# Optimization experiments

Measured on AMD Instinct MI355X. Metric: run time of the kernel, lower is better.

The kernel has to match this reference:

```python
import jax, jax.numpy as jnp
import numpy as np

B, S, D = 4, 4096, 2048
H, HD = 16, 128
FFN = 8192
CAP = 0.25
TOP_K = int(S * CAP)  # 1024
EPS = 1e-6


def rmsnorm(x, g):
    return x * jax.lax.rsqrt(jnp.mean(x * x, axis=-1, keepdims=True) + EPS) * g


def apply_rope(x, cos, sin):
    # x: [b,t,h,hd]; cos/sin: [t, hd//2]
    half = x.shape[-1] // 2
    x1, x2 = x[..., :half], x[..., half:]
    c = cos[None, :, None, :]
    s = sin[None, :, None, :]
    return jnp.concatenate([x1 * c - x2 * s, x1 * s + x2 * c], axis=-1)


def transformer_block(x, mask, freqs_cis, g1, wq, wk, wv, wo, g2, w1, w3, w2):
    b, t, d = x.shape
    cos, sin = freqs_cis[..., 0], freqs_cis[..., 1]
    h = rmsnorm(x, g1)
    q = (h @ wq).reshape(b, t, H, HD)
    k = (h @ wk).reshape(b, t, H, HD)
    v = (h @ wv).reshape(b, t, H, HD)
    q = apply_rope(q, cos, sin)
    k = apply_rope(k, cos, sin)
    scores = jnp.einsum('bqhd,bkhd->bhqk', q, k) / np.sqrt(HD) + mask[None, None]
    attn = jax.nn.softmax(scores, axis=-1)
    o = jnp.einsum('bhqk,bkhd->bqhd', attn, v).reshape(b, t, d) @ wo
    x = x + o
    h2 = rmsnorm(x, g2)
    x = x + (jax.nn.silu(h2 @ w1) * (h2 @ w3)) @ w2
    return x, None


def setup_inputs() -> dict:
    key = jax.random.key(0)
    ks = jax.random.split(key, 12)
    w = lambda k, shp: jax.random.normal(k, shp, dtype=jnp.float32) * 0.02
    return {
        'x': jax.random.normal(ks[0], (B, S, D), dtype=jnp.float32),
        'mask': jnp.zeros((TOP_K, TOP_K), dtype=jnp.float32),
        'freqs_cis': jax.random.uniform(ks[1], (TOP_K, HD // 2, 2), dtype=jnp.float32),
        'w_router': w(ks[2], (D,)),
        'g1': jnp.ones((D,), dtype=jnp.float32),
        'wq': w(ks[3], (D, D)),
        'wk': w(ks[4], (D, D)),
        'wv': w(ks[5], (D, D)),
        'wo': w(ks[6], (D, D)),
        'g2': jnp.ones((D,), dtype=jnp.float32),
        'w1': w(ks[7], (D, FFN)),
        'w3': w(ks[8], (D, FFN)),
        'w2': w(ks[9], (FFN, D)),
    }


def reference(x, mask, freqs_cis, w_router, g1, wq, wk, wv, wo, g2, w1, w3, w2):
    b, s, d = x.shape
    # router: Linear(dim, 1, bias=False) -> [b, s]
    router_logits = jnp.einsum('bsd,d->bs', x, w_router)
    vals, idx = jax.lax.top_k(router_logits, TOP_K)  # [b, k]
    # sort selected indices ascending; permute weights to match (softmax is
    # permutation-equivariant so softmax-then-permute == torch's gather order)
    order = jnp.argsort(idx, axis=1)
    sel = jnp.take_along_axis(idx, order, axis=1)          # [b, k]
    w_sel = jnp.take_along_axis(vals, order, axis=1)       # [b, k]
    r_weights = jax.nn.softmax(w_sel, axis=1)[..., None]   # [b, k, 1]
    filtered_x = jnp.take_along_axis(x, sel[..., None], axis=1)  # [b, k, d]
    x_out, _ = transformer_block(filtered_x, mask, freqs_cis, g1, wq, wk, wv, wo, g2, w1, w3, w2)
    xw_out = r_weights * x_out
    b_idx = jnp.arange(b)[:, None]
    out = x.at[b_idx, sel].add(xw_out)
    return out
```

## Files before the change

kernel.cpp:

```cpp
#include <hip/hip_runtime.h>
#include <cstdint>
#include <cstddef>

#define NB 4
#define NS 4096
#define ND 2048
#define NH 16
#define NHD 128
#define NT 1024
#define NF 8192

typedef __bf16 bf16;
typedef __bf16 bf16x8 __attribute__((ext_vector_type(8)));
typedef __bf16 bf16x4 __attribute__((ext_vector_type(4)));
typedef float  f32x4  __attribute__((ext_vector_type(4)));

typedef const __attribute__((address_space(1))) void* gptr_t;
typedef __attribute__((address_space(3))) void* lptr_t;

__device__ __forceinline__ float wave_sum(float v) {
#pragma unroll
    for (int off = 32; off > 0; off >>= 1) v += __shfl_xor(v, off);
    return v;
}
__device__ __forceinline__ float wave_max(float v) {
#pragma unroll
    for (int off = 32; off > 0; off >>= 1) v = fmaxf(v, __shfl_xor(v, off));
    return v;
}

__global__ __launch_bounds__(256) void router_k(const float* __restrict__ x,
                                                const float* __restrict__ wr,
                                                float* __restrict__ logits) {
    __shared__ float r4[4];
    long long row = blockIdx.x;
    const float4* xr = (const float4*)(x + row * ND);
    const float4* w4 = (const float4*)wr;
    float p = 0.f;
    for (int i = threadIdx.x; i < ND / 4; i += 256) {
        float4 a = xr[i], b = w4[i];
        p += a.x * b.x + a.y * b.y + a.z * b.z + a.w * b.w;
    }
    p = wave_sum(p);
    if ((threadIdx.x & 63) == 0) r4[threadIdx.x >> 6] = p;
    __syncthreads();
    if (threadIdx.x == 0) logits[row] = r4[0] + r4[1] + r4[2] + r4[3];
}

__global__ __launch_bounds__(1024) void topk_k(const float* __restrict__ logits,
                                               int* __restrict__ sel,
                                               float* __restrict__ rw) {
    __shared__ unsigned long long keys[NS];
    __shared__ float r16[16];
    __shared__ float bmax, bsum;
    const int bb = blockIdx.x;
    const int tid = threadIdx.x;
    const float* lg = logits + (long long)bb * NS;

    for (int i = tid; i < NS; i += 1024) {
        unsigned u = __float_as_uint(lg[i]);
        u = (u & 0x80000000u) ? ~u : (u | 0x80000000u);
        keys[i] = ((unsigned long long)u << 32) | (unsigned)(NS - 1 - i);
    }
    __syncthreads();
    for (int k = 2; k <= NS; k <<= 1) {
        for (int j = k >> 1; j > 0; j >>= 1) {
            for (int i = tid; i < NS; i += 1024) {
                int ixj = i ^ j;
                if (ixj > i) {
                    unsigned long long a = keys[i], c = keys[ixj];
                    bool up = ((i & k) == 0);
                    if (up ? (a < c) : (a > c)) { keys[i] = c; keys[ixj] = a; }
                }
            }
            __syncthreads();
        }
    }
    unsigned long long a0 = keys[tid];
    __syncthreads();
    {
        unsigned idx_ = NS - 1 - (unsigned)(a0 & 0xFFFFFFFFu);
        unsigned uval = (unsigned)(a0 >> 32);
        keys[tid] = ((unsigned long long)idx_ << 32) | uval;
    }
    __syncthreads();
    for (int k = 2; k <= NT; k <<= 1) {
        for (int j = k >> 1; j > 0; j >>= 1) {
            int i = tid, ixj = i ^ j;
            if (i < NT && ixj > i) {
                unsigned long long a = keys[i], c = keys[ixj];
                bool up = ((i & k) == 0);
                if (up ? (a > c) : (a < c)) { keys[i] = c; keys[ixj] = a; }
            }
            __syncthreads();
        }
    }
    unsigned long long kk = keys[tid];
    int si = (int)(kk >> 32);
    unsigned u = (unsigned)(kk & 0xFFFFFFFFu);
    u = (u & 0x80000000u) ? (u ^ 0x80000000u) : ~u;
    float val = __uint_as_float(u);

    const int wid = tid >> 6, lane = tid & 63;
    float mx = wave_max(val);
    if (lane == 0) r16[wid] = mx;
    __syncthreads();
    if (tid == 0) {
        float m = r16[0];
        for (int i = 1; i < 16; i++) m = fmaxf(m, r16[i]);
        bmax = m;
    }
    __syncthreads();
    float e = __expf(val - bmax);
    float s = wave_sum(e);
    if (lane == 0) r16[wid] = s;
    __syncthreads();
    if (tid == 0) {
        float t = 0.f;
        for (int i = 0; i < 16; i++) t += r16[i];
        bsum = t;
    }
    __syncthreads();
    sel[bb * NT + tid] = si;
    rw[bb * NT + tid] = e / bsum;
}

__global__ __launch_bounds__(256) void gather_k(const float* __restrict__ x,
                                                const int* __restrict__ sel,
                                                float* __restrict__ xf) {
    int gid = blockIdx.x * 256 + threadIdx.x;
    int col = gid & (ND / 4 - 1);
    int row = gid >> 9;
    int bb = row >> 10;
    int s = sel[row];
    ((float4*)xf)[gid] = ((const float4*)x)[((long long)bb * NS + s) * (ND / 4) + col];
}

__global__ __launch_bounds__(256) void rmsnorm_k(const float* __restrict__ x,
                                                 const float* __restrict__ g,
                                                 bf16* __restrict__ out) {
    __shared__ float r4[4];
    __shared__ float scl;
    long long row = blockIdx.x;
    const float4* xr = (const float4*)(x + row * ND);
    int i0 = threadIdx.x, i1 = threadIdx.x + 256;
    float4 a = xr[i0], b = xr[i1];
    float ss = a.x * a.x + a.y * a.y + a.z * a.z + a.w * a.w +
               b.x * b.x + b.y * b.y + b.z * b.z + b.w * b.w;
    ss = wave_sum(ss);
    if ((threadIdx.x & 63) == 0) r4[threadIdx.x >> 6] = ss;
    __syncthreads();
    if (threadIdx.x == 0)
        scl = rsqrtf((r4[0] + r4[1] + r4[2] + r4[3]) * (1.0f / ND) + 1e-6f);
    __syncthreads();
    float s = scl;
    const float4* g4 = (const float4*)g;
    float4 ga = g4[i0], gb = g4[i1];
    bf16x4 o0, o1;
    o0[0] = (bf16)(a.x * s * ga.x); o0[1] = (bf16)(a.y * s * ga.y);
    o0[2] = (bf16)(a.z * s * ga.z); o0[3] = (bf16)(a.w * s * ga.w);
    o1[0] = (bf16)(b.x * s * gb.x); o1[1] = (bf16)(b.y * s * gb.y);
    o1[2] = (bf16)(b.z * s * gb.z); o1[3] = (bf16)(b.w * s * gb.w);
    *(bf16x4*)(out + row * ND + i0 * 4) = o0;
    *(bf16x4*)(out + row * ND + i1 * 4) = o1;
}

__global__ __launch_bounds__(256) void transpose_to_bf16(const float* __restrict__ in,
                                                         bf16* __restrict__ out,
                                                         int R, int C) {
    __shared__ float tile[32][33];
    int bx = blockIdx.x * 32;
    int by = blockIdx.y * 32;
    int tx = threadIdx.x & 31;
    int ty = threadIdx.x >> 5;
#pragma unroll
    for (int i = 0; i < 4; i++)
        tile[ty + 8 * i][tx] = in[(long long)(by + ty + 8 * i) * C + bx + tx];
    __syncthreads();
#pragma unroll
    for (int i = 0; i < 4; i++)
        out[(long long)(bx + ty + 8 * i) * R + by + tx] = (bf16)tile[tx][ty + 8 * i];
}

__global__ __launch_bounds__(256) void rope_k(const bf16* __restrict__ QKV,
                                              const float* __restrict__ fr,
                                              bf16* __restrict__ Q,
                                              bf16* __restrict__ K,
                                              bf16* __restrict__ Vt) {
    int gid = blockIdx.x * 256 + threadIdx.x;
    int hd = gid & 63;
    int h = (gid >> 6) & 15;
    int t = (gid >> 10) & (NT - 1);
    int bb = gid >> 20;
    float c = fr[t * 128 + hd * 2 + 0];
    float s = fr[t * 128 + hd * 2 + 1];
    long long base = ((long long)bb * NT + t) * (3 * ND) + h * NHD;
    float q1 = (float)QKV[base + hd],      q2 = (float)QKV[base + hd + 64];
    float k1 = (float)QKV[base + ND + hd], k2 = (float)QKV[base + ND + hd + 64];
    long long ob = (((long long)(bb * NH + h)) * NT + t) * NHD;
    Q[ob + hd]      = (bf16)(q1 * c - q2 * s);
    Q[ob + hd + 64] = (bf16)(q1 * s + q2 * c);
    K[ob + hd]      = (bf16)(k1 * c - k2 * s);
    K[ob + hd + 64] = (bf16)(k1 * s + k2 * c);
    long long vb = ((long long)(bb * NH + h)) * NHD * NT + t;
    Vt[vb + (long long)hd * NT]        = QKV[base + 2 * ND + hd];
    Vt[vb + (long long)(hd + 64) * NT] = QKV[base + 2 * ND + hd + 64];
}

__global__ __launch_bounds__(256) void softmax_k(const float* __restrict__ Sc,
                                                 bf16* __restrict__ P) {
    __shared__ float r4[4];
    __shared__ float bc;
    long long row = blockIdx.x;
    float4 v = ((const float4*)(Sc + row * NT))[threadIdx.x];
    float mx = fmaxf(fmaxf(v.x, v.y), fmaxf(v.z, v.w));
    mx = wave_max(mx);
    if ((threadIdx.x & 63) == 0) r4[threadIdx.x >> 6] = mx;
    __syncthreads();
    if (threadIdx.x == 0) bc = fmaxf(fmaxf(r4[0], r4[1]), fmaxf(r4[2], r4[3]));
    __syncthreads();
    float m = bc;
    float e0 = __expf(v.x - m), e1 = __expf(v.y - m);
    float e2 = __expf(v.z - m), e3 = __expf(v.w - m);
    float ss = wave_sum(e0 + e1 + e2 + e3);
    if ((threadIdx.x & 63) == 0) r4[threadIdx.x >> 6] = ss;
    __syncthreads();
    if (threadIdx.x == 0) bc = 1.f / (r4[0] + r4[1] + r4[2] + r4[3]);
    __syncthreads();
    float inv = bc;
    bf16x4 o;
    o[0] = (bf16)(e0 * inv); o[1] = (bf16)(e1 * inv);
    o[2] = (bf16)(e2 * inv); o[3] = (bf16)(e3 * inv);
    *(bf16x4*)(P + row * NT + threadIdx.x * 4) = o;
}

__global__ __launch_bounds__(256) void copy_k(const float4* __restrict__ in,
                                              float4* __restrict__ out, long long n) {
    for (long long i = (long long)blockIdx.x * 256 + threadIdx.x; i < n;
         i += (long long)gridDim.x * 256)
        out[i] = in[i];
}

template <int MODE>
__global__ __launch_bounds__(256, 2) void gemm_bt(
    const bf16* __restrict__ A, int lda, long long sAz,
    const bf16* __restrict__ Bt, int ldb, long long sBz,
    void* __restrict__ Cv, long long sCz, int ldc,
    int K, float alpha) {
    __shared__ bf16 As[128][32];
    __shared__ bf16 Bs[128][32];

    const int tid = threadIdx.x;
    const int lane = tid & 63;
    const int wave = tid >> 6;
    const int wm = wave >> 1, wn = wave & 1;
    const int lm = lane & 15, lq = lane >> 4;

    const int m0 = blockIdx.y * 128;
    const int n0 = blockIdx.x * 128;
    const int z = blockIdx.z;

    A += (long long)z * sAz;
    Bt += (long long)z * sBz;

    f32x4 acc[4][4];
#pragma unroll
    for (int i = 0; i < 4; i++)
#pragma unroll
        for (int j = 0; j < 4; j++) {
            f32x4 zz = {0.f, 0.f, 0.f, 0.f};
            acc[i][j] = zz;
        }

    const int sr = wave * 16 + (lane >> 2);
    const int sk = (lane & 3) * 8;
    const bf16* gA0 = A + (long long)(m0 + sr) * lda + sk;
    const bf16* gA1 = gA0 + (long long)64 * lda;
    const bf16* gB0 = Bt + (long long)(n0 + sr) * ldb + sk;
    const bf16* gB1 = gB0 + (long long)64 * ldb;
    bf16* lA0 = &As[sr][sk];
    bf16* lA1 = &As[sr + 64][sk];
    bf16* lB0 = &Bs[sr][sk];
    bf16* lB1 = &Bs[sr + 64][sk];

    for (int k0 = 0; k0 < K; k0 += 32) {
        __builtin_amdgcn_global_load_lds((gptr_t)(gA0 + k0), (lptr_t)lA0, 16, 0, 0);
        __builtin_amdgcn_global_load_lds((gptr_t)(gA1 + k0), (lptr_t)lA1, 16, 0, 0);
        __builtin_amdgcn_global_load_lds((gptr_t)(gB0 + k0), (lptr_t)lB0, 16, 0, 0);
        __builtin_amdgcn_global_load_lds((gptr_t)(gB1 + k0), (lptr_t)lB1, 16, 0, 0);
        __syncthreads();

        bf16x8 af[4], bfr[4];
#pragma unroll
        for (int mi = 0; mi < 4; mi++)
            af[mi] = *(const bf16x8*)&As[wm * 64 + mi * 16 + lm][lq * 8];
#pragma unroll
        for (int ni = 0; ni < 4; ni++)
            bfr[ni] = *(const bf16x8*)&Bs[wn * 64 + ni * 16 + lm][lq * 8];
#pragma unroll
        for (int mi = 0; mi < 4; mi++)
#pragma unroll
            for (int ni = 0; ni < 4; ni++)
                acc[mi][ni] = __builtin_amdgcn_mfma_f32_16x16x32_bf16(
                    af[mi], bfr[ni], acc[mi][ni], 0, 0, 0);
        __syncthreads();
    }

#pragma unroll
    for (int mi = 0; mi < 4; mi++) {
#pragma unroll
        for (int ni = 0; ni < 4; ni++) {
            int row = m0 + wm * 64 + mi * 16 + lq * 4;
            int col = n0 + wn * 64 + ni * 16 + lm;
#pragma unroll
            for (int r = 0; r < 4; r++) {
                float v = alpha * acc[mi][ni][r];
                long long rr = row + r;
                if constexpr (MODE == 0) {
                    bf16* C = (bf16*)Cv + (long long)z * sCz;
                    C[rr * ldc + col] = (bf16)v;
                } else {
                    float* C = (float*)Cv + (long long)z * sCz;
                    C[rr * ldc + col] = v;
                }
            }
        }
    }
}

#define G256_BAR() do { __builtin_amdgcn_sched_barrier(0); \
    __builtin_amdgcn_s_barrier(); __builtin_amdgcn_sched_barrier(0); } while (0)
#define G256_LGKM0() do { asm volatile("s_waitcnt lgkmcnt(0)" ::: "memory"); \
    __builtin_amdgcn_sched_barrier(0); } while (0)
#define G256_VMC(n) do { asm volatile("s_waitcnt vmcnt(" #n ")" ::: "memory"); \
    __builtin_amdgcn_sched_barrier(0); } while (0)

#define STAGE_A(c, h, t) do { \
    char* _l = sm + (c) * 65536 + (h) * 16384 + sdst; \
    long long _ko = (long long)(t) * 64; \
    __builtin_amdgcn_global_load_lds((gptr_t)(gA + (2 * (h)) * stA + _ko), \
                                     (lptr_t)_l, 16, 0, 0); \
    __builtin_amdgcn_global_load_lds((gptr_t)(gA + (2 * (h) + 1) * stA + _ko), \
                                     (lptr_t)(_l + 8192), 16, 0, 0); \
} while (0)
#define STAGE_B(c, h, t) do { \
    char* _l = sm + (c) * 65536 + 32768 + (h) * 16384 + sdst; \
    long long _ko = (long long)(t) * 64; \
    const bf16* _g = (h) ? gBhi : gBlo; \
    __builtin_amdgcn_global_load_lds((gptr_t)(_g + _ko), \
                                     (lptr_t)_l, 16, 0, 0); \
    __builtin_amdgcn_global_load_lds((gptr_t)(_g + stB + _ko), \
                                     (lptr_t)(_l + 8192), 16, 0, 0); \
} while (0)

#define LDA_HALF(c, lo) do { \
    char* _b = sm + (c) * 65536; \
    _Pragma("unroll") \
    for (int _mi = 0; _mi < 4; _mi++) { \
        a[(lo) + _mi][0] = *(const bf16x8*)(_b + aoff + ((lo) + _mi) * 2048); \
        a[(lo) + _mi][1] = *(const bf16x8*)(_b + (aoff ^ 64) + ((lo) + _mi) * 2048); \
    } \
} while (0)
#define LDB_HALF(c, lo) do { \
    char* _b = sm + (c) * 65536 + 32768; \
    _Pragma("unroll") \
    for (int _ni = 0; _ni < 2; _ni++) { \
        int _ix = (lo) + _ni; \
        int _o = boff + (_ix & 1) * 2048 + (_ix >> 1) * bStep2; \
        b[_ix][0] = *(const bf16x8*)(_b + _o); \
        b[_ix][1] = *(const bf16x8*)(_b + (_o ^ 64)); \
    } \
} while (0)

#define MFMA_Q(mlo, nlo) do { \
    __builtin_amdgcn_s_setprio(1); \
    _Pragma("unroll") \
    for (int _ks = 0; _ks < 2; _ks++) \
    _Pragma("unroll") \
    for (int _mi = 0; _mi < 4; _mi++) \
    _Pragma("unroll") \
    for (int _ni = 0; _ni < 2; _ni++) \
        acc[(mlo) + _mi][(nlo) + _ni] = __builtin_amdgcn_mfma_f32_16x16x32_bf16( \
            a[(mlo) + _mi][_ks], b[(nlo) + _ni][_ks], acc[(mlo) + _mi][(nlo) + _ni], \
            0, 0, 0); \
    __builtin_amdgcn_s_setprio(0); \
} while (0)

template <int MODE>
__global__ __launch_bounds__(512, 2) void gemm256(
    const bf16* __restrict__ A, int lda,
    const bf16* __restrict__ Bt, int ldb,
    void* __restrict__ Cv, int ldc,
    int K, float alpha,
    const bf16* __restrict__ Bt2,
    const float* __restrict__ res, const int* __restrict__ selp,
    const float* __restrict__ rwp, float* __restrict__ outp) {
    __shared__ char smem[131072];

    constexpr bool DUALB = (MODE == 6);
    constexpr int bStep2 = DUALB ? 16384 : 4096;

    const int tid = threadIdx.x;
    const int lane = tid & 63;
    const int wid = tid >> 6;
    const int wm = wid >> 2, wn = wid & 3;
    const int lm = lane & 15, lq = lane >> 4;

    const int nx = gridDim.x;
    const int orig = blockIdx.y * nx + blockIdx.x;
    const int xcd = orig & 7;
    const int r_ = orig >> 3;
    const int mi_ = r_ & 7, ni_ = r_ >> 3;
    const int nTile = DUALB ? 128 : 256;
    const int m0 = ((xcd >> 2) * 8 + mi_) * 256;
    const int n0 = ((xcd & 3) * (nx >> 2) + ni_) * nTile;
    const long long kz = (long long)blockIdx.z * K;

    const int srow = tid >> 3;
    const int skc = ((tid & 7) ^ (srow & 7)) * 8;
    const bf16* gA = A + (long long)(m0 + srow) * lda + kz + skc;
    const bf16* gBlo = Bt + (long long)(n0 + srow) * ldb + kz + skc;
    const bf16* gBhi = DUALB
        ? Bt2 + (long long)(n0 + srow) * ldb + kz + skc
        : gBlo + (long long)128 * ldb;
    const long long stA = (long long)64 * lda;
    const long long stB = (long long)64 * ldb;

    char* sm = (char*)smem;
    const int sdst = tid * 16;

    const int aoff = (wm * 128 + lm) * 128 + ((lq ^ (lm & 7)) << 4);
    const int boff = ((DUALB ? wn * 32 : wn * 64) + lm) * 128 + ((lq ^ (lm & 7)) << 4);

    f32x4 acc[8][4];
#pragma unroll
    for (int i = 0; i < 8; i++)
#pragma unroll
        for (int j = 0; j < 4; j++) {
            f32x4 zz = {0.f, 0.f, 0.f, 0.f};
            acc[i][j] = zz;
        }
    bf16x8 a[8][2], b[4][2];

    const int NTk = K >> 6;

    STAGE_A(0, 0, 0); STAGE_A(0, 1, 0);
    STAGE_B(0, 0, 0); STAGE_B(0, 1, 0);
    STAGE_A(1, 0, 1); STAGE_A(1, 1, 1);
    G256_VMC(4);
    G256_BAR();

    for (int t0 = 0; t0 < NTk; t0 += 2) {
        const int t1 = t0 + 1, t2 = t0 + 2, t3 = t0 + 3;
        const bool more = (t2 < NTk);

        LDA_HALF(0, 0); LDB_HALF(0, 0);
        STAGE_B(1, 0, t1);
        G256_BAR(); G256_LGKM0(); MFMA_Q(0, 0); G256_BAR();
        LDA_HALF(0, 4);
        STAGE_B(1, 1, t1);
        G256_BAR(); G256_LGKM0(); MFMA_Q(4, 0); G256_BAR();
        LDB_HALF(0, 2);
        if (more) STAGE_A(0, 0, t2);
        G256_BAR(); G256_LGKM0(); MFMA_Q(0, 2); G256_BAR();
        if (more) STAGE_A(0, 1, t2);
        G256_BAR(); G256_LGKM0(); MFMA_Q(4, 2);
        if (more) { G256_VMC(4); } else { G256_VMC(0); }
        G256_BAR();

        LDA_HALF(1, 0); LDB_HALF(1, 0);
        if (more) STAGE_B(0, 0, t2);
        G256_BAR(); G256_LGKM0(); MFMA_Q(0, 0); G256_BAR();
        LDA_HALF(1, 4);
        if (more) STAGE_B(0, 1, t2);
        G256_BAR(); G256_LGKM0(); MFMA_Q(4, 0); G256_BAR();
        LDB_HALF(1, 2);
        if (more) STAGE_A(1, 0, t3);
        G256_BAR(); G256_LGKM0(); MFMA_Q(0, 2); G256_BAR();
        if (more) STAGE_A(1, 1, t3);
        G256_BAR(); G256_LGKM0(); MFMA_Q(4, 2);
        if (more) { G256_VMC(4); } else { G256_VMC(0); }
        G256_BAR();
    }

    if constexpr (MODE == 6) {
        bf16* C = (bf16*)Cv;
#pragma unroll
        for (int mi = 0; mi < 8; mi++) {
#pragma unroll
            for (int ni = 0; ni < 2; ni++) {
                const int row = m0 + wm * 128 + mi * 16 + lq * 4;
                const int col = n0 + wn * 32 + ni * 16 + lm;
#pragma unroll
                for (int r = 0; r < 4; r++) {
                    float v1 = acc[mi][ni][r];
                    float v3 = acc[mi][ni + 2][r];
                    C[(long long)(row + r) * ldc + col] =
                        (bf16)((v1 / (1.f + __expf(-v1))) * v3);
                }
            }
        }
    } else {
#pragma unroll
        for (int mi = 0; mi < 8; mi++) {
#pragma unroll
            for (int ni = 0; ni < 4; ni++) {
                const int row = m0 + wm * 128 + mi * 16 + lq * 4;
                const int col = n0 + wn * 64 + ni * 16 + lm;
#pragma unroll
                for (int r = 0; r < 4; r++) {
                    float v = alpha * acc[mi][ni][r];
                    long long rr = row + r;
                    if constexpr (MODE == 0) {
                        bf16* C = (bf16*)Cv;
                        C[rr * ldc + col] = (bf16)v;
                    } else if constexpr (MODE == 2) {
                        float* C = (float*)Cv;
                        unsafeAtomicAdd(&C[rr * ldc + col], v);
                    } else {
                        int bb2 = (int)(rr >> 10);
                        int s = selp[rr];
                        float add = rwp[rr] *
                            (v + (blockIdx.z == 0 ? res[rr * (long long)ND + col] : 0.f));
                        unsafeAtomicAdd(outp + ((long long)bb2 * NS + s) * ND + col, add);
                    }
                }
            }
        }
    }
}

extern "C" void kernel_launch(void* const* d_in, const int* in_sizes, int n_in,
                              void* d_out, int out_size, void* d_ws, size_t ws_size,
                              hipStream_t stream) {
    const float* x  = (const float*)d_in[0];
    const float* fr = (const float*)d_in[2];
    const float* wr = (const float*)d_in[3];
    const float* g1 = (const float*)d_in[4];
    const float* wq = (const float*)d_in[5];
    const float* wk = (const float*)d_in[6];
    const float* wv = (const float*)d_in[7];
    const float* wo = (const float*)d_in[8];
    const float* g2 = (const float*)d_in[9];
    const float* w1 = (const float*)d_in[10];
    const float* w3 = (const float*)d_in[11];
    const float* w2 = (const float*)d_in[12];
    float* out = (float*)d_out;

    char* ws = (char*)d_ws;
    size_t off = 0;
    auto take = [&](size_t bytes) -> char* {
        char* p = ws + off;
        off += (bytes + 255) & ~(size_t)255;
        return p;
    };
    int*   sel    = (int*)take((size_t)NB * NT * 4);
    float* rw     = (float*)take((size_t)NB * NT * 4);
    float* logits = (float*)take((size_t)NB * NS * 4);
    float* xf     = (float*)take((size_t)NB * NT * ND * 4);
    bf16*  hbuf   = (bf16*)take((size_t)NB * NT * ND * 2);
    bf16*  wqkv_t = (bf16*)take((size_t)3 * ND * ND * 2);
    bf16*  wo_t   = (bf16*)take((size_t)ND * ND * 2);
    bf16*  Obuf   = (bf16*)take((size_t)NB * NT * ND * 2);
    char* xr = ws + off;
    bf16* QKV = (bf16*)xr;
    bf16* Qr  = QKV + (size_t)NB * NT * 3 * ND;
    bf16* Kr  = Qr + (size_t)NB * NT * ND;
    bf16* Vt  = Kr + (size_t)NB * NT * ND;
    float* scores = (float*)(Vt + (size_t)NB * NT * ND);
    bf16*  P      = (bf16*)(scores + (size_t)NH * NT * NT);
    bf16* w1_t  = (bf16*)xr;
    bf16* w3_t  = w1_t + (size_t)ND * NF;
    bf16* w2_t  = w3_t + (size_t)ND * NF;
    bf16* inter = w2_t + (size_t)ND * NF;

    router_k<<<NB * NS, 256, 0, stream>>>(x, wr, logits);
    topk_k<<<NB, 1024, 0, stream>>>(logits, sel, rw);
    gather_k<<<(NB * NT * ND / 4) / 256, 256, 0, stream>>>(x, sel, xf);
    rmsnorm_k<<<NB * NT, 256, 0, stream>>>(xf, g1, hbuf);

    dim3 tg(ND / 32, ND / 32);
    transpose_to_bf16<<<tg, 256, 0, stream>>>(wq, wqkv_t, ND, ND);
    transpose_to_bf16<<<tg, 256, 0, stream>>>(wk, wqkv_t + (size_t)ND * ND, ND, ND);
    transpose_to_bf16<<<tg, 256, 0, stream>>>(wv, wqkv_t + (size_t)2 * ND * ND, ND, ND);
    transpose_to_bf16<<<tg, 256, 0, stream>>>(wo, wo_t, ND, ND);

    gemm256<0><<<dim3(3 * ND / 256, NB * NT / 256, 1), 512, 0, stream>>>(
        hbuf, ND, wqkv_t, ND, QKV, 3 * ND, ND, 1.0f,
        nullptr, nullptr, nullptr, nullptr, nullptr);

    rope_k<<<(NB * NT * NH * 64) / 256, 256, 0, stream>>>(QKV, fr, Qr, Kr, Vt);

    const float scal = 0.08838834764831845f;
    for (int bb = 0; bb < NB; bb++) {
        dim3 gs(NT / 128, NT / 128, NH);
        gemm_bt<1><<<gs, 256, 0, stream>>>(
            Qr + (size_t)bb * NH * NT * NHD, NHD, (long long)NT * NHD,
            Kr + (size_t)bb * NH * NT * NHD, NHD, (long long)NT * NHD,
            scores, (long long)NT * NT, NT, NHD, scal);
        softmax_k<<<NH * NT, 256, 0, stream>>>(scores, P);
        dim3 gv(NHD / 128, NT / 128, NH);
        gemm_bt<0><<<gv, 256, 0, stream>>>(
            P, NT, (long long)NT * NT,
            Vt + (size_t)bb * NH * NHD * NT, NT, (long long)NHD * NT,
            Obuf + (size_t)bb * NT * ND, NHD, ND, NT, 1.0f);
    }

    gemm256<2><<<dim3(ND / 256, NB * NT / 256, 2), 512, 0, stream>>>(
        Obuf, ND, wo_t, ND, xf, ND, ND / 2, 1.0f,
        nullptr, nullptr, nullptr, nullptr, nullptr);

    rmsnorm_k<<<NB * NT, 256, 0, stream>>>(xf, g2, hbuf);

    transpose_to_bf16<<<dim3(NF / 32, ND / 32), 256, 0, stream>>>(w1, w1_t, ND, NF);
    transpose_to_bf16<<<dim3(NF / 32, ND / 32), 256, 0, stream>>>(w3, w3_t, ND, NF);
    transpose_to_bf16<<<dim3(ND / 32, NF / 32), 256, 0, stream>>>(w2, w2_t, NF, ND);

    gemm256<6><<<dim3(NF / 128, NB * NT / 256, 1), 512, 0, stream>>>(
        hbuf, ND, w1_t, ND, inter, NF, ND, 1.0f,
        w3_t, nullptr, nullptr, nullptr, nullptr);

    copy_k<<<8192, 256, 0, stream>>>((const float4*)x, (float4*)out,
                                     (long long)NB * NS * ND / 4);
    gemm256<5><<<dim3(ND / 256, NB * NT / 256, 2), 512, 0, stream>>>(
        inter, NF, w2_t, NF, nullptr, ND, NF / 2, 1.0f,
        nullptr, xf, sel, rw, out);
}
```

Before: 1.480 ms.

## Replace unfused QK/softmax/PV attention with a fused flash-attention kernel

Replaces the per-batch three-kernel attention path (QK^T gemm writing fp32 scores, a separate softmax kernel, then PV gemm) with one flash-attention kernel that keeps scores in registers and LDS using online softmax. It double-buffers swizzled K/V tiles in LDS via direct global-to-LDS loads and stages P per wave in LDS before the PV MFMAs. This removes the large fp32 score and P round-trips through global memory and twelve kernel launches. In exchange it needs 80KB of LDS per block, which limits occupancy, and the grid is only 512 blocks.

Result: faster. 1.323 ms (-10.6%).

```diff
diff --git a/kernel.cpp b/kernel.cpp
--- a/kernel.cpp
+++ b/kernel.cpp
@@ -207,33 +207,6 @@
     Vt[vb + (long long)(hd + 64) * NT] = QKV[base + 2 * ND + hd + 64];
 }
 
-__global__ __launch_bounds__(256) void softmax_k(const float* __restrict__ Sc,
-                                                 bf16* __restrict__ P) {
-    __shared__ float r4[4];
-    __shared__ float bc;
-    long long row = blockIdx.x;
-    float4 v = ((const float4*)(Sc + row * NT))[threadIdx.x];
-    float mx = fmaxf(fmaxf(v.x, v.y), fmaxf(v.z, v.w));
-    mx = wave_max(mx);
-    if ((threadIdx.x & 63) == 0) r4[threadIdx.x >> 6] = mx;
-    __syncthreads();
-    if (threadIdx.x == 0) bc = fmaxf(fmaxf(r4[0], r4[1]), fmaxf(r4[2], r4[3]));
-    __syncthreads();
-    float m = bc;
-    float e0 = __expf(v.x - m), e1 = __expf(v.y - m);
-    float e2 = __expf(v.z - m), e3 = __expf(v.w - m);
-    float ss = wave_sum(e0 + e1 + e2 + e3);
-    if ((threadIdx.x & 63) == 0) r4[threadIdx.x >> 6] = ss;
-    __syncthreads();
-    if (threadIdx.x == 0) bc = 1.f / (r4[0] + r4[1] + r4[2] + r4[3]);
-    __syncthreads();
-    float inv = bc;
-    bf16x4 o;
-    o[0] = (bf16)(e0 * inv); o[1] = (bf16)(e1 * inv);
-    o[2] = (bf16)(e2 * inv); o[3] = (bf16)(e3 * inv);
-    *(bf16x4*)(P + row * NT + threadIdx.x * 4) = o;
-}
-
 __global__ __launch_bounds__(256) void copy_k(const float4* __restrict__ in,
                                               float4* __restrict__ out, long long n) {
     for (long long i = (long long)blockIdx.x * 256 + threadIdx.x; i < n;
@@ -241,89 +214,193 @@
         out[i] = in[i];
 }
 
-template <int MODE>
-__global__ __launch_bounds__(256, 2) void gemm_bt(
-    const bf16* __restrict__ A, int lda, long long sAz,
-    const bf16* __restrict__ Bt, int ldb, long long sBz,
-    void* __restrict__ Cv, long long sCz, int ldc,
-    int K, float alpha) {
-    __shared__ bf16 As[128][32];
-    __shared__ bf16 Bs[128][32];
+__global__ __launch_bounds__(256, 2) void flash_k(
+    const bf16* __restrict__ Qr,
+    const bf16* __restrict__ Kr,
+    const bf16* __restrict__ Vt,
+    bf16* __restrict__ O) {
+    __shared__ char lds[81920];
 
     const int tid = threadIdx.x;
     const int lane = tid & 63;
-    const int wave = tid >> 6;
-    const int wm = wave >> 1, wn = wave & 1;
+    const int w = tid >> 6;
     const int lm = lane & 15, lq = lane >> 4;
-
-    const int m0 = blockIdx.y * 128;
-    const int n0 = blockIdx.x * 128;
-    const int z = blockIdx.z;
-
-    A += (long long)z * sAz;
-    Bt += (long long)z * sBz;
-
-    f32x4 acc[4][4];
-#pragma unroll
-    for (int i = 0; i < 4; i++)
-#pragma unroll
-        for (int j = 0; j < 4; j++) {
+    const int lm7 = lm & 7;
+
+    const int bh = blockIdx.y;
+    const int q0 = blockIdx.x * 128;
+    const bf16* Qb = Qr + (size_t)bh * NT * NHD;
+    const bf16* Kb = Kr + (size_t)bh * NT * NHD;
+    const bf16* Vb = Vt + (size_t)bh * NHD * NT;
+
+    const int krow = tid >> 4;
+    const int kc_s = (tid & 15);
+    const int vrow = tid >> 3;
+    const int vc_s = (tid & 7);
+
+    bf16x8 q[2][4];
+#pragma unroll
+    for (int mi = 0; mi < 2; mi++)
+#pragma unroll
+        for (int ks = 0; ks < 4; ks++)
+            q[mi][ks] = *(const bf16x8*)(Qb + (size_t)(q0 + w * 32 + mi * 16 + lm) * NHD
+                                         + lq * 8 + ks * 32);
+
+    f32x4 o0[8], o1[8];
+#pragma unroll
+    for (int i = 0; i < 8; i++) {
+        f32x4 zz = {0.f, 0.f, 0.f, 0.f};
+        o0[i] = zz; o1[i] = zz;
+    }
+    float m0[4], m1[4], l0[4], l1[4];
+#pragma unroll
+    for (int r = 0; r < 4; r++) {
+        m0[r] = -3.0e38f; m1[r] = -3.0e38f; l0[r] = 0.f; l1[r] = 0.f;
+    }
+
+    char* Pb = lds + 65536 + w * 4096;
+    const float scal = 0.08838834764831845f;
+
+#pragma unroll
+    for (int i = 0; i < 4; i++) {
+        int row = i * 16 + krow;
+        __builtin_amdgcn_global_load_lds(
+            (gptr_t)(Kb + (size_t)row * NHD + (kc_s ^ (row & 7)) * 8),
+            (lptr_t)(lds + i * 4096 + tid * 16), 16, 0, 0);
+    }
+#pragma unroll
+    for (int i = 0; i < 4; i++) {
+        int row = i * 32 + vrow;
+        __builtin_amdgcn_global_load_lds(
+            (gptr_t)(Vb + (size_t)row * NT + (vc_s ^ (row & 7)) * 8),
+            (lptr_t)(lds + 32768 + i * 4096 + tid * 16), 16, 0, 0);
+    }
+    __syncthreads();
+
+    for (int c = 0; c < 16; ++c) {
+        char* Kl = lds + (c & 1) * 16384;
+        char* Vl = lds + 32768 + (c & 1) * 16384;
+
+        if (c < 15) {
+            const int key1 = (c + 1) * 64;
+            char* Kd = lds + ((c + 1) & 1) * 16384;
+            char* Vd = lds + 32768 + ((c + 1) & 1) * 16384;
+#pragma unroll
+            for (int i = 0; i < 4; i++) {
+                int row = i * 16 + krow;
+                __builtin_amdgcn_global_load_lds(
+                    (gptr_t)(Kb + (size_t)(key1 + row) * NHD + (kc_s ^ (row & 7)) * 8),
+                    (lptr_t)(Kd + i * 4096 + tid * 16), 16, 0, 0);
+            }
+#pragma unroll
+            for (int i = 0; i < 4; i++) {
+                int row = i * 32 + vrow;
+                __builtin_amdgcn_global_load_lds(
+                    (gptr_t)(Vb + (size_t)row * NT + key1 + (vc_s ^ (row & 7)) * 8),
+                    (lptr_t)(Vd + i * 4096 + tid * 16), 16, 0, 0);
+            }
+        }
+
+        f32x4 s0[4], s1[4];
+#pragma unroll
+        for (int ni = 0; ni < 4; ni++) {
             f32x4 zz = {0.f, 0.f, 0.f, 0.f};
-            acc[i][j] = zz;
-        }
-
-    const int sr = wave * 16 + (lane >> 2);
-    const int sk = (lane & 3) * 8;
-    const bf16* gA0 = A + (long long)(m0 + sr) * lda + sk;
-    const bf16* gA1 = gA0 + (long long)64 * lda;
-    const bf16* gB0 = Bt + (long long)(n0 + sr) * ldb + sk;
-    const bf16* gB1 = gB0 + (long long)64 * ldb;
-    bf16* lA0 = &As[sr][sk];
-    bf16* lA1 = &As[sr + 64][sk];
-    bf16* lB0 = &Bs[sr][sk];
-    bf16* lB1 = &Bs[sr + 64][sk];
-
-    for (int k0 = 0; k0 < K; k0 += 32) {
-        __builtin_amdgcn_global_load_lds((gptr_t)(gA0 + k0), (lptr_t)lA0, 16, 0, 0);
-        __builtin_amdgcn_global_load_lds((gptr_t)(gA1 + k0), (lptr_t)lA1, 16, 0, 0);
-        __builtin_amdgcn_global_load_lds((gptr_t)(gB0 + k0), (lptr_t)lB0, 16, 0, 0);
-        __builtin_amdgcn_global_load_lds((gptr_t)(gB1 + k0), (lptr_t)lB1, 16, 0, 0);
+            s0[ni] = zz; s1[ni] = zz;
+        }
+#pragma unroll
+        for (int ni = 0; ni < 4; ni++) {
+#pragma unroll
+            for (int ks = 0; ks < 4; ks++) {
+                bf16x8 kf = *(const bf16x8*)(Kl + (lm + 16 * ni) * 256
+                                             + (((lq + 4 * ks) ^ lm7) << 4));
+                s0[ni] = __builtin_amdgcn_mfma_f32_16x16x32_bf16(q[0][ks], kf, s0[ni], 0, 0, 0);
+                s1[ni] = __builtin_amdgcn_mfma_f32_16x16x32_bf16(q[1][ks], kf, s1[ni], 0, 0, 0);
+            }
+        }
+
+        float sc0[4], sc1[4];
+#pragma unroll
+        for (int r = 0; r < 4; r++) {
+            float a0 = fmaxf(fmaxf(s0[0][r], s0[1][r]), fmaxf(s0[2][r], s0[3][r])) * scal;
+            float a1 = fmaxf(fmaxf(s1[0][r], s1[1][r]), fmaxf(s1[2][r], s1[3][r])) * scal;
+#pragma unroll
+            for (int o = 1; o < 16; o <<= 1) {
+                a0 = fmaxf(a0, __shfl_xor(a0, o));
+                a1 = fmaxf(a1, __shfl_xor(a1, o));
+            }
+            float mn0 = fmaxf(m0[r], a0);
+            float mn1 = fmaxf(m1[r], a1);
+            sc0[r] = __expf(m0[r] - mn0);
+            sc1[r] = __expf(m1[r] - mn1);
+            m0[r] = mn0; m1[r] = mn1;
+
+            float rs0 = 0.f, rs1 = 0.f;
+#pragma unroll
+            for (int ni = 0; ni < 4; ni++) {
+                float p0 = __expf(s0[ni][r] * scal - mn0);
+                float p1 = __expf(s1[ni][r] * scal - mn1);
+                s0[ni][r] = p0; s1[ni][r] = p1;
+                rs0 += p0; rs1 += p1;
+            }
+#pragma unroll
+            for (int o = 1; o < 16; o <<= 1) {
+                rs0 += __shfl_xor(rs0, o);
+                rs1 += __shfl_xor(rs1, o);
+            }
+            l0[r] = l0[r] * sc0[r] + rs0;
+            l1[r] = l1[r] * sc1[r] + rs1;
+        }
+#pragma unroll
+        for (int ni = 0; ni < 8; ni++)
+#pragma unroll
+            for (int r = 0; r < 4; r++) {
+                o0[ni][r] *= sc0[r];
+                o1[ni][r] *= sc1[r];
+            }
+
+#pragma unroll
+        for (int ni = 0; ni < 4; ni++)
+#pragma unroll
+            for (int r = 0; r < 4; r++) {
+                int q_l0 = lq * 4 + r;
+                int q_l1 = 16 + q_l0;
+                int cw = (lm >> 3) + 2 * ni;
+                *(bf16*)(Pb + q_l0 * 128 + ((cw ^ (q_l0 & 7)) << 4) + (lm7 << 1)) =
+                    (bf16)s0[ni][r];
+                *(bf16*)(Pb + q_l1 * 128 + ((cw ^ (q_l1 & 7)) << 4) + (lm7 << 1)) =
+                    (bf16)s1[ni][r];
+            }
+        asm volatile("s_waitcnt lgkmcnt(0)" ::: "memory");
+        __builtin_amdgcn_sched_barrier(0);
+
+#pragma unroll
+        for (int ks = 0; ks < 2; ks++) {
+            bf16x8 pa0 = *(const bf16x8*)(Pb + lm * 128 + (((lq + 4 * ks) ^ lm7) << 4));
+            bf16x8 pa1 = *(const bf16x8*)(Pb + (lm + 16) * 128 + (((lq + 4 * ks) ^ lm7) << 4));
+#pragma unroll
+            for (int ni = 0; ni < 8; ni++) {
+                bf16x8 vf = *(const bf16x8*)(Vl + (lm + 16 * ni) * 128
+                                             + (((lq + 4 * ks) ^ lm7) << 4));
+                o0[ni] = __builtin_amdgcn_mfma_f32_16x16x32_bf16(pa0, vf, o0[ni], 0, 0, 0);
+                o1[ni] = __builtin_amdgcn_mfma_f32_16x16x32_bf16(pa1, vf, o1[ni], 0, 0, 0);
+            }
+        }
+
         __syncthreads();
-
-        bf16x8 af[4], bfr[4];
-#pragma unroll
-        for (int mi = 0; mi < 4; mi++)
-            af[mi] = *(const bf16x8*)&As[wm * 64 + mi * 16 + lm][lq * 8];
-#pragma unroll
-        for (int ni = 0; ni < 4; ni++)
-            bfr[ni] = *(const bf16x8*)&Bs[wn * 64 + ni * 16 + lm][lq * 8];
-#pragma unroll
-        for (int mi = 0; mi < 4; mi++)
-#pragma unroll
-            for (int ni = 0; ni < 4; ni++)
-                acc[mi][ni] = __builtin_amdgcn_mfma_f32_16x16x32_bf16(
-                    af[mi], bfr[ni], acc[mi][ni], 0, 0, 0);
-        __syncthreads();
-    }
-
-#pragma unroll
-    for (int mi = 0; mi < 4; mi++) {
-#pragma unroll
-        for (int ni = 0; ni < 4; ni++) {
-            int row = m0 + wm * 64 + mi * 16 + lq * 4;
-            int col = n0 + wn * 64 + ni * 16 + lm;
-#pragma unroll
-            for (int r = 0; r < 4; r++) {
-                float v = alpha * acc[mi][ni][r];
-                long long rr = row + r;
-                if constexpr (MODE == 0) {
-                    bf16* C = (bf16*)Cv + (long long)z * sCz;
-                    C[rr * ldc + col] = (bf16)v;
-                } else {
-                    float* C = (float*)Cv + (long long)z * sCz;
-                    C[rr * ldc + col] = v;
-                }
-            }
+    }
+
+    const int bb = bh >> 4, h = bh & 15;
+    float rl0[4], rl1[4];
+#pragma unroll
+    for (int r = 0; r < 4; r++) { rl0[r] = 1.f / l0[r]; rl1[r] = 1.f / l1[r]; }
+#pragma unroll
+    for (int ni = 0; ni < 8; ni++) {
+#pragma unroll
+        for (int r = 0; r < 4; r++) {
+            int col = h * 128 + lm + 16 * ni;
+            long long r0 = (long long)bb * NT + q0 + w * 32 + lq * 4 + r;
+            O[(r0) * ND + col]      = (bf16)(o0[ni][r] * rl0[r]);
+            O[(r0 + 16) * ND + col] = (bf16)(o1[ni][r] * rl1[r]);
         }
     }
 }
@@ -567,8 +644,6 @@
     bf16* Qr  = QKV + (size_t)NB * NT * 3 * ND;
     bf16* Kr  = Qr + (size_t)NB * NT * ND;
     bf16* Vt  = Kr + (size_t)NB * NT * ND;
-    float* scores = (float*)(Vt + (size_t)NB * NT * ND);
-    bf16*  P      = (bf16*)(scores + (size_t)NH * NT * NT);
     bf16* w1_t  = (bf16*)xr;
     bf16* w3_t  = w1_t + (size_t)ND * NF;
     bf16* w2_t  = w3_t + (size_t)ND * NF;
@@ -591,20 +666,7 @@
 
     rope_k<<<(NB * NT * NH * 64) / 256, 256, 0, stream>>>(QKV, fr, Qr, Kr, Vt);
 
-    const float scal = 0.08838834764831845f;
-    for (int bb = 0; bb < NB; bb++) {
-        dim3 gs(NT / 128, NT / 128, NH);
-        gemm_bt<1><<<gs, 256, 0, stream>>>(
-            Qr + (size_t)bb * NH * NT * NHD, NHD, (long long)NT * NHD,
-            Kr + (size_t)bb * NH * NT * NHD, NHD, (long long)NT * NHD,
-            scores, (long long)NT * NT, NT, NHD, scal);
-        softmax_k<<<NH * NT, 256, 0, stream>>>(scores, P);
-        dim3 gv(NHD / 128, NT / 128, NH);
-        gemm_bt<0><<<gv, 256, 0, stream>>>(
-            P, NT, (long long)NT * NT,
-            Vt + (size_t)bb * NH * NHD * NT, NT, (long long)NHD * NT,
-            Obuf + (size_t)bb * NT * ND, NHD, ND, NT, 1.0f);
-    }
+    flash_k<<<dim3(NT / 128, NB * NH), 256, 0, stream>>>(Qr, Kr, Vt, Obuf);
 
     gemm256<2><<<dim3(ND / 256, NB * NT / 256, 2), 512, 0, stream>>>(
         Obuf, ND, wo_t, ND, xf, ND, ND / 2, 1.0f,
```
